# Performance work log

Measured on AMD Instinct MI355X. Metric: run time of the kernel, lower is better.

The kernel has to match this reference:

```python
import jax, jax.numpy as jnp
import numpy as np

N, F, M, B = 100000, 256, 10, 32768
DECAY = 0.9


def setup_inputs() -> dict:
    key = jax.random.key(0)
    ks = jax.random.split(key, 16)
    s = 1.0 / np.sqrt(F)
    # forward args
    node_indices = jax.random.permutation(ks[0], N)[:B]  # unique indices
    node_features = jax.random.normal(ks[1], (B, F), jnp.float32)
    # per-node state
    hidden_states = jax.random.normal(ks[2], (N, F), jnp.float32) * 0.1
    cell_states = jax.random.normal(ks[3], (N, F), jnp.float32) * 0.1
    temporal_memory = jax.random.normal(ks[4], (N, M, F), jnp.float32) * 0.1
    memory_ptr = jax.random.randint(ks[5], (N,), 0, M)
    # LSTMCell params (gate order i, f, g, o as in torch)
    W_ih = jax.random.normal(ks[6], (4 * F, F), jnp.float32) * s
    W_hh = jax.random.normal(ks[7], (4 * F, F), jnp.float32) * s
    b_ih = jax.random.normal(ks[8], (4 * F,), jnp.float32) * s
    b_hh = jax.random.normal(ks[9], (4 * F,), jnp.float32) * s
    # attention read params
    Wq = jax.random.normal(ks[10], (F, F), jnp.float32) * s
    bq = jnp.zeros((F,), jnp.float32)
    Wk = jax.random.normal(ks[11], (F, F), jnp.float32) * s
    bk = jnp.zeros((F,), jnp.float32)
    Wv = jax.random.normal(ks[12], (F, F), jnp.float32) * s
    bv = jnp.zeros((F,), jnp.float32)
    return dict(node_indices=node_indices, node_features=node_features,
                hidden_states=hidden_states, cell_states=cell_states,
                temporal_memory=temporal_memory, memory_ptr=memory_ptr,
                W_ih=W_ih, W_hh=W_hh, b_ih=b_ih, b_hh=b_hh,
                Wq=Wq, bq=bq, Wk=Wk, bk=bk, Wv=Wv, bv=bv)


def reference(node_indices, node_features, hidden_states, cell_states,
              temporal_memory, memory_ptr, W_ih, W_hh, b_ih, b_hh,
              Wq, bq, Wk, bk, Wv, bv):
    idx = node_indices
    feat = node_features.shape[-1]
    # --- update_memory: LSTMCell on gathered per-node states ---
    h_prev = hidden_states[idx]              # (B, F)
    c_prev = cell_states[idx]                # (B, F)
    gates = node_features @ W_ih.T + b_ih + h_prev @ W_hh.T + b_hh
    i, f, g, o = jnp.split(gates, 4, axis=-1)
    c_new = jax.nn.sigmoid(f) * c_prev + jax.nn.sigmoid(i) * jnp.tanh(g)
    h_new = jax.nn.sigmoid(o) * jnp.tanh(c_new)
    # --- scatter into circular temporal memory + decay previous slot ---
    ptr = memory_ptr[idx]                    # (B,)
    tm = temporal_memory.at[idx, ptr].set(node_features)
    prev = ptr - 1                           # -1 wraps; decay only applied if ptr > 0
    old = tm[idx, prev]                      # (B, F)
    tm = tm.at[idx, prev].set(jnp.where((ptr > 0)[:, None], old * DECAY, old))
    # --- get_temporal_context: gather + tiny attention over M slots ---
    mem = tm[idx]                            # (B, M, F)
    q = h_new @ Wq.T + bq                    # (B, F)  hidden_states[idx] post-update == h_new
    k = mem @ Wk.T + bk                      # (B, M, F)
    v = mem @ Wv.T + bv                      # (B, M, F)
    scores = jnp.einsum('bf,bmf->bm', q, k) / jnp.sqrt(jnp.asarray(feat, q.dtype))
    w = jax.nn.softmax(scores, axis=-1)      # (B, M)
    context = jnp.einsum('bmf,bm->bf', v, w) # (B, F)
    return context
```

## Files before the change

kernel.cpp:

```cpp
#include <hip/hip_runtime.h>
#include <hip/hip_bf16.h>

constexpr int NB = 32768;
constexpr int NF = 256;
constexpr int NM = 10;
constexpr float DECAY = 0.9f;

using bf16x8 = __attribute__((ext_vector_type(8))) short;
using f32x4  = __attribute__((ext_vector_type(4))) float;

static __device__ __forceinline__ ushort f2bf(float x) {
    unsigned u = __float_as_uint(x);
    unsigned r = (u + 0x7fffu + ((u >> 16) & 1u)) >> 16;
    return (ushort)r;
}
static __device__ __forceinline__ float bf2f(ushort x) {
    return __uint_as_float(((unsigned)x) << 16);
}
static __device__ __forceinline__ float sigmoid_f(float x) {
    return 1.f / (1.f + __expf(-x));
}
static __device__ __forceinline__ float tanh_f(float x) {
    float e = __expf(2.f * x);
    return (e - 1.f) / (e + 1.f);
}
static __device__ __forceinline__ void gload16(const void* g, void* l) {
    __builtin_amdgcn_global_load_lds(
        (const __attribute__((address_space(1))) unsigned int*)g,
        (__attribute__((address_space(3))) unsigned int*)l, 16, 0, 0);
}


__global__ void k_build_wgi(const float* __restrict__ W_ih, const float* __restrict__ W_hh,
                            const float* __restrict__ b_ih, const float* __restrict__ b_hh,
                            ushort* __restrict__ Wgi, float* __restrict__ bsum) {
    int j = blockIdx.x;
    int f = j >> 2, g = j & 3;
    int sr = g * 256 + f;
    for (int c = threadIdx.x; c < 512; c += 256) {
        float v = (c < 256) ? W_ih[sr * 256 + c] : W_hh[sr * 256 + (c - 256)];
        Wgi[j * 512 + c] = f2bf(v);
    }
    if (threadIdx.x == 0) bsum[j] = b_ih[sr] + b_hh[sr];
}

__global__ void k_build_wqkt(const float* __restrict__ Wq, const float* __restrict__ Wk,
                             ushort* __restrict__ WqkT) {
    int i = blockIdx.x, a = threadIdx.x;
    float s = 0.f;
#pragma unroll 8
    for (int j = 0; j < 256; ++j) s += Wq[j * 256 + a] * Wk[j * 256 + i];
    WqkT[i * 256 + a] = f2bf(s * 0.0625f);
}

__global__ void k_build_bqk(const float* __restrict__ bq, const float* __restrict__ Wk,
                            float* __restrict__ bqk) {
    int i = threadIdx.x;
    float s = 0.f;
#pragma unroll 8
    for (int j = 0; j < 256; ++j) s += bq[j] * Wk[j * 256 + i];
    bqk[i] = s * 0.0625f;
}

__global__ void k_conv_wv(const float* __restrict__ Wv, ushort* __restrict__ Wvb) {
    int t = blockIdx.x * 256 + threadIdx.x;
    Wvb[t] = f2bf(Wv[t]);
}

__global__ void k_build_acat(const float* __restrict__ nf, const float* __restrict__ hidden,
                             const int* __restrict__ idx, ushort* __restrict__ Acat) {
    int t = blockIdx.x * 256 + threadIdx.x;
    int row = t >> 7;
    int c4 = (t & 127) * 4;
    const float* src = (c4 < 256) ? (nf + (long)row * 256 + c4)
                                  : (hidden + (long)idx[row] * 256 + (c4 - 256));
    float4 v = *reinterpret_cast<const float4*>(src);
    ushort4 o;
    o.x = f2bf(v.x); o.y = f2bf(v.y); o.z = f2bf(v.z); o.w = f2bf(v.w);
    *reinterpret_cast<ushort4*>(Acat + (long)row * 512 + c4) = o;
}

__global__ __launch_bounds__(256) void k_gates2(
    const ushort* __restrict__ Acat, const ushort* __restrict__ Wgi,
    const float* __restrict__ bsum, const int* __restrict__ idx,
    const float* __restrict__ cell, ushort* __restrict__ h_new)
{
    __shared__ ushort As[128 * 32];
    __shared__ ushort Bs[128 * 32];
    const int t = threadIdx.x;
    const int w = t >> 6, l = t & 63;
    const int wr = w >> 1, wc = w & 1;
    const int lr = l & 15, lk = l >> 4;
    const int row0 = blockIdx.x * 128;
    const int col0 = blockIdx.y * 128;

    f32x4 acc[4][4];
#pragma unroll
    for (int m = 0; m < 4; ++m)
#pragma unroll
        for (int n = 0; n < 4; ++n) acc[m][n] = f32x4{0.f, 0.f, 0.f, 0.f};

    const int srow = l >> 2;
    const int scol = (l & 3) * 8;
    const int u0 = w * 2, u1 = u0 + 1;
    const ushort* aS0 = Acat + (size_t)(row0 + u0 * 16 + srow) * 512 + scol;
    const ushort* aS1 = Acat + (size_t)(row0 + u1 * 16 + srow) * 512 + scol;
    const ushort* bS0 = Wgi  + (size_t)(col0 + u0 * 16 + srow) * 512 + scol;
    const ushort* bS1 = Wgi  + (size_t)(col0 + u1 * 16 + srow) * 512 + scol;
    ushort* aL0 = As + u0 * 512; ushort* aL1 = As + u1 * 512;
    ushort* bL0 = Bs + u0 * 512; ushort* bL1 = Bs + u1 * 512;

    for (int k0 = 0; k0 < 512; k0 += 32) {
        gload16(aS0 + k0, aL0);
        gload16(aS1 + k0, aL1);
        gload16(bS0 + k0, bL0);
        gload16(bS1 + k0, bL1);
        __syncthreads();
        bf16x8 af[4], bfr[4];
#pragma unroll
        for (int m = 0; m < 4; ++m)
            af[m] = *reinterpret_cast<const bf16x8*>(As + (wr * 64 + m * 16 + lr) * 32 + lk * 8);
#pragma unroll
        for (int n = 0; n < 4; ++n)
            bfr[n] = *reinterpret_cast<const bf16x8*>(Bs + (wc * 64 + n * 16 + lr) * 32 + lk * 8);
#pragma unroll
        for (int m = 0; m < 4; ++m)
#pragma unroll
            for (int n = 0; n < 4; ++n)
                acc[m][n] = __builtin_amdgcn_mfma_f32_16x16x32_bf16(af[m], bfr[n], acc[m][n], 0, 0, 0);
        __syncthreads();
    }

    float bb[4];
#pragma unroll
    for (int n = 0; n < 4; ++n) bb[n] = bsum[col0 + wc * 64 + n * 16 + lr];
#pragma unroll
    for (int m = 0; m < 4; ++m)
#pragma unroll
        for (int n = 0; n < 4; ++n)
#pragma unroll
            for (int r = 0; r < 4; ++r) acc[m][n][r] += bb[n];

    const int g0 = lr & 3;
    const int fq = lr >> 2;
    const bool is0 = (g0 == 0), is1 = (g0 == 1), is2 = (g0 == 2), is3 = (g0 == 3);
    const int fbase = (col0 >> 2) + wc * 16;

    int nodev[4];
#pragma unroll
    for (int r = 0; r < 4; ++r)
        nodev[r] = idx[row0 + wr * 64 + g0 * 16 + lk * 4 + r];

#pragma unroll
    for (int n = 0; n < 4; ++n) {
#pragma unroll
        for (int r = 0; r < 4; ++r) {
            float own = is0 ? acc[0][n][r] : is1 ? acc[1][n][r] : is2 ? acc[2][n][r] : acc[3][n][r];
            float s1  = is0 ? acc[1][n][r] : is1 ? acc[0][n][r] : is2 ? acc[3][n][r] : acc[2][n][r];
            float s2  = is0 ? acc[2][n][r] : is1 ? acc[3][n][r] : is2 ? acc[0][n][r] : acc[1][n][r];
            float s3  = is0 ? acc[3][n][r] : is1 ? acc[2][n][r] : is2 ? acc[1][n][r] : acc[0][n][r];
            float r1 = __shfl_xor(s1, 1, 64);
            float r2 = __shfl_xor(s2, 2, 64);
            float r3 = __shfl_xor(s3, 3, 64);
            float gi = is0 ? own : is1 ? r1 : is2 ? r2 : r3;
            float gf = is1 ? own : is0 ? r1 : is3 ? r2 : r3;
            float gg = is2 ? own : is3 ? r1 : is0 ? r2 : r3;
            float go = is3 ? own : is2 ? r1 : is1 ? r2 : r3;
            int fg = fbase + n * 4 + fq;
            float cp = cell[(size_t)nodev[r] * 256 + fg];
            float cn = sigmoid_f(gf) * cp + sigmoid_f(gi) * tanh_f(gg);
            float hn = sigmoid_f(go) * tanh_f(cn);
            int grow = row0 + wr * 64 + g0 * 16 + lk * 4 + r;
            h_new[(size_t)grow * 256 + fg] = f2bf(hn);
        }
    }
}

static __device__ __forceinline__ int swzb(int row, int byteInRow) {
    return (row * 512 + byteInRow) ^ ((row & 7) << 4);
}

__global__ __launch_bounds__(256) void k_tail(
    const ushort* __restrict__ hnew, const ushort* __restrict__ WqkT,
    const float* __restrict__ bqk, const ushort* __restrict__ Wvb,
    const float* __restrict__ bv,
    const int* __restrict__ idx, const int* __restrict__ mptr,
    const float* __restrict__ tm, const float* __restrict__ nf,
    float* __restrict__ out)
{
    __shared__ ushort sQ[64 * 256];
    const int t = threadIdx.x, w = t >> 6, l = t & 63;
    const int lr = l & 15, lk = l >> 4;
    const int row0 = blockIdx.x * 64;
    char* sB = (char*)sQ;

    f32x4 acc[4][4];
#pragma unroll
    for (int m = 0; m < 4; ++m)
#pragma unroll
        for (int n = 0; n < 4; ++n) acc[m][n] = f32x4{0.f, 0.f, 0.f, 0.f};

    const ushort* aptr[4];
#pragma unroll
    for (int m = 0; m < 4; ++m) aptr[m] = hnew + (size_t)(row0 + m * 16 + lr) * 256 + lk * 8;
    const ushort* bptr[4];
#pragma unroll
    for (int n = 0; n < 4; ++n) bptr[n] = WqkT + (size_t)(w * 64 + n * 16 + lr) * 256 + lk * 8;

#pragma unroll 2
    for (int k = 0; k < 256; k += 32) {
        bf16x8 a[4], b[4];
#pragma unroll
        for (int m = 0; m < 4; ++m) a[m] = *reinterpret_cast<const bf16x8*>(aptr[m] + k);
#pragma unroll
        for (int n = 0; n < 4; ++n) b[n] = *reinterpret_cast<const bf16x8*>(bptr[n] + k);
#pragma unroll
        for (int m = 0; m < 4; ++m)
#pragma unroll
            for (int n = 0; n < 4; ++n)
                acc[m][n] = __builtin_amdgcn_mfma_f32_16x16x32_bf16(a[m], b[n], acc[m][n], 0, 0, 0);
    }
#pragma unroll
    for (int m = 0; m < 4; ++m)
#pragma unroll
        for (int n = 0; n < 4; ++n) {
            int colc = w * 64 + n * 16 + lr;
            float bbq = bqk[colc];
#pragma unroll
            for (int r = 0; r < 4; ++r) {
                int row = m * 16 + lk * 4 + r;
                *(ushort*)(sB + swzb(row, colc * 2)) = f2bf(acc[m][n][r] + bbq);
            }
        }
    __syncthreads();

    for (int rr = 0; rr < 16; ++rr) {
        int row = w * 16 + rr;
        int b = row0 + row;
        int node = idx[b];
        int ptr = mptr[node];
        ushort4 q4 = *(const ushort4*)(sB + swzb(row, l * 8));
        float q0 = bf2f(q4.x), q1 = bf2f(q4.y), q2 = bf2f(q4.z), q3 = bf2f(q4.w);
        const float* base = tm + (size_t)node * (NM * NF);

        float4 mem[NM];
        float sc[NM];
#pragma unroll
        for (int m = 0; m < NM; ++m) {
            float4 v;
            if (m == ptr) {
                v = *reinterpret_cast<const float4*>(nf + (size_t)b * 256 + l * 4);
            } else {
                v = *reinterpret_cast<const float4*>(base + (size_t)m * 256 + l * 4);
                if (ptr > 0 && m == ptr - 1) { v.x *= DECAY; v.y *= DECAY; v.z *= DECAY; v.w *= DECAY; }
            }
            mem[m] = v;
            sc[m] = q0 * v.x + q1 * v.y + q2 * v.z + q3 * v.w;
        }
#pragma unroll
        for (int m = 0; m < NM; ++m) {
            float s = sc[m];
#pragma unroll
            for (int d = 1; d < 64; d <<= 1) s += __shfl_xor(s, d, 64);
            sc[m] = s;
        }
        float mx = sc[0];
#pragma unroll
        for (int m = 1; m < NM; ++m) mx = fmaxf(mx, sc[m]);
        float e[NM], sum = 0.f;
#pragma unroll
        for (int m = 0; m < NM; ++m) { e[m] = __expf(sc[m] - mx); sum += e[m]; }
        float inv = 1.f / sum;

        float4 c = {0.f, 0.f, 0.f, 0.f};
#pragma unroll
        for (int m = 0; m < NM; ++m) {
            float wm = e[m] * inv;
            c.x += wm * mem[m].x; c.y += wm * mem[m].y; c.z += wm * mem[m].z; c.w += wm * mem[m].w;
        }
        ushort4 o;
        o.x = f2bf(c.x); o.y = f2bf(c.y); o.z = f2bf(c.z); o.w = f2bf(c.w);
        *(ushort4*)(sB + swzb(row, l * 8)) = o;
    }
    __syncthreads();

#pragma unroll
    for (int m = 0; m < 4; ++m)
#pragma unroll
        for (int n = 0; n < 4; ++n) acc[m][n] = f32x4{0.f, 0.f, 0.f, 0.f};
    const ushort* vptr[4];
#pragma unroll
    for (int n = 0; n < 4; ++n) vptr[n] = Wvb + (size_t)(w * 64 + n * 16 + lr) * 256 + lk * 8;

#pragma unroll 2
    for (int k = 0; k < 256; k += 32) {
        bf16x8 a[4], b[4];
#pragma unroll
        for (int m = 0; m < 4; ++m)
            a[m] = *reinterpret_cast<const bf16x8*>(sB + swzb(m * 16 + lr, (k + lk * 8) * 2));
#pragma unroll
        for (int n = 0; n < 4; ++n) b[n] = *reinterpret_cast<const bf16x8*>(vptr[n] + k);
#pragma unroll
        for (int m = 0; m < 4; ++m)
#pragma unroll
            for (int n = 0; n < 4; ++n)
                acc[m][n] = __builtin_amdgcn_mfma_f32_16x16x32_bf16(a[m], b[n], acc[m][n], 0, 0, 0);
    }
#pragma unroll
    for (int m = 0; m < 4; ++m)
#pragma unroll
        for (int n = 0; n < 4; ++n) {
            int colc = w * 64 + n * 16 + lr;
            float bbv = bv[colc];
#pragma unroll
            for (int r = 0; r < 4; ++r) {
                int row = m * 16 + lk * 4 + r;
                out[(size_t)(row0 + row) * 256 + colc] = acc[m][n][r] + bbv;
            }
        }
}

extern "C" void kernel_launch(void* const* d_in, const int* in_sizes, int n_in,
                              void* d_out, int out_size, void* d_ws, size_t ws_size,
                              hipStream_t stream) {
    const int*   node_indices = (const int*)  d_in[0];
    const float* node_feats   = (const float*)d_in[1];
    const float* hidden       = (const float*)d_in[2];
    const float* cell         = (const float*)d_in[3];
    const float* tmem         = (const float*)d_in[4];
    const int*   memory_ptr   = (const int*)  d_in[5];
    const float* W_ih         = (const float*)d_in[6];
    const float* W_hh         = (const float*)d_in[7];
    const float* b_ih         = (const float*)d_in[8];
    const float* b_hh         = (const float*)d_in[9];
    const float* Wq           = (const float*)d_in[10];
    const float* bq           = (const float*)d_in[11];
    const float* Wk           = (const float*)d_in[12];
    const float* Wv           = (const float*)d_in[14];
    const float* bv           = (const float*)d_in[15];

    char* ws = (char*)d_ws;
    size_t off = 0;
    auto alloc = [&](size_t bytes) { char* p = ws + off; off += (bytes + 255) & ~(size_t)255; return p; };

    ushort* Wgi   = (ushort*)alloc((size_t)1024 * 512 * 2);
    ushort* WqkT  = (ushort*)alloc((size_t)256 * 256 * 2);
    ushort* Wvb   = (ushort*)alloc((size_t)256 * 256 * 2);
    float*  bqk   = (float*) alloc((size_t)256 * 4);
    float*  bsum  = (float*) alloc((size_t)1024 * 4);
    ushort* Acat  = (ushort*)alloc((size_t)NB * 512 * 2);
    ushort* hnew  = (ushort*)alloc((size_t)NB * 256 * 2);

    k_build_wgi <<<1024, 256, 0, stream>>>(W_ih, W_hh, b_ih, b_hh, Wgi, bsum);
    k_build_wqkt<<<256, 256, 0, stream>>>(Wq, Wk, WqkT);
    k_build_bqk <<<1, 256, 0, stream>>>(bq, Wk, bqk);
    k_conv_wv   <<<256, 256, 0, stream>>>(Wv, Wvb);
    k_build_acat<<<NB * 128 / 256, 256, 0, stream>>>(node_feats, hidden, node_indices, Acat);

    k_gates2<<<dim3(NB / 128, 8), 256, 0, stream>>>(Acat, Wgi, bsum, node_indices, cell, hnew);
    k_tail  <<<NB / 64, 256, 0, stream>>>(hnew, WqkT, bqk, Wvb, bv,
                                          node_indices, memory_ptr, tmem, node_feats,
                                          (float*)d_out);
}
```

Before: 224.2 us.

## Merge prep kernels into one launch and halve tail kernel rows per block

Fuses the five preprocessing kernels (weight conversions, Wq·Wk fold, bias fold, Acat gather) into a single block-dispatched kernel, cutting launch overhead. The tail kernel now processes 32 rows per block instead of 64. That doubles the grid for more occupancy and latency hiding on the gather-heavy attention stage, and halves shared memory. Node indices and memory pointers are now prefetched per wave before the attention loop. The trade-off is that the Wqk and Wv weight tiles are reloaded twice as often across blocks.

```diff
diff --git a/kernel.cpp b/kernel.cpp
--- a/kernel.cpp
+++ b/kernel.cpp
@@ -30,54 +30,59 @@
         (__attribute__((address_space(3))) unsigned int*)l, 16, 0, 0);
 }
 
-
-__global__ void k_build_wgi(const float* __restrict__ W_ih, const float* __restrict__ W_hh,
-                            const float* __restrict__ b_ih, const float* __restrict__ b_hh,
-                            ushort* __restrict__ Wgi, float* __restrict__ bsum) {
-    int j = blockIdx.x;
-    int f = j >> 2, g = j & 3;
-    int sr = g * 256 + f;
-    for (int c = threadIdx.x; c < 512; c += 256) {
-        float v = (c < 256) ? W_ih[sr * 256 + c] : W_hh[sr * 256 + (c - 256)];
-        Wgi[j * 512 + c] = f2bf(v);
-    }
-    if (threadIdx.x == 0) bsum[j] = b_ih[sr] + b_hh[sr];
-}
-
-__global__ void k_build_wqkt(const float* __restrict__ Wq, const float* __restrict__ Wk,
-                             ushort* __restrict__ WqkT) {
-    int i = blockIdx.x, a = threadIdx.x;
-    float s = 0.f;
+constexpr int PB_ACAT = 16384;
+constexpr int PB_WGI  = PB_ACAT + 1024;
+constexpr int PB_WQKT = PB_WGI + 256;
+constexpr int PB_WV   = PB_WQKT + 256;
+constexpr int PB_TOT  = PB_WV + 1;
+
+__global__ __launch_bounds__(256) void k_prep(
+    const float* __restrict__ W_ih, const float* __restrict__ W_hh,
+    const float* __restrict__ b_ih, const float* __restrict__ b_hh,
+    const float* __restrict__ Wq, const float* __restrict__ bq,
+    const float* __restrict__ Wk, const float* __restrict__ Wv,
+    const float* __restrict__ nf, const float* __restrict__ hidden,
+    const int* __restrict__ idx,
+    ushort* __restrict__ Wgi, float* __restrict__ bsum,
+    ushort* __restrict__ WqkT, float* __restrict__ bqk,
+    ushort* __restrict__ Wvb, ushort* __restrict__ Acat)
+{
+    const int blk = blockIdx.x, tid = threadIdx.x;
+    if (blk < PB_ACAT) {
+        int t = blk * 256 + tid;
+        int row = t >> 7;
+        int c4 = (t & 127) * 4;
+        const float* src = (c4 < 256) ? (nf + (size_t)row * 256 + c4)
+                                      : (hidden + (size_t)idx[row] * 256 + (c4 - 256));
+        float4 v = *reinterpret_cast<const float4*>(src);
+        ushort4 o;
+        o.x = f2bf(v.x); o.y = f2bf(v.y); o.z = f2bf(v.z); o.w = f2bf(v.w);
+        *reinterpret_cast<ushort4*>(Acat + (size_t)row * 512 + c4) = o;
+    } else if (blk < PB_WGI) {
+        int j = blk - PB_ACAT;
+        int f = j >> 2, g = j & 3;
+        int sr = g * 256 + f;
+        for (int c = tid; c < 512; c += 256) {
+            float v = (c < 256) ? W_ih[sr * 256 + c] : W_hh[sr * 256 + (c - 256)];
+            Wgi[j * 512 + c] = f2bf(v);
+        }
+        if (tid == 0) bsum[j] = b_ih[sr] + b_hh[sr];
+    } else if (blk < PB_WQKT) {
+        int i = blk - PB_WGI, a = tid;
+        float s = 0.f;
 #pragma unroll 8
-    for (int j = 0; j < 256; ++j) s += Wq[j * 256 + a] * Wk[j * 256 + i];
-    WqkT[i * 256 + a] = f2bf(s * 0.0625f);
-}
-
-__global__ void k_build_bqk(const float* __restrict__ bq, const float* __restrict__ Wk,
-                            float* __restrict__ bqk) {
-    int i = threadIdx.x;
-    float s = 0.f;
+        for (int j = 0; j < 256; ++j) s += Wq[j * 256 + a] * Wk[j * 256 + i];
+        WqkT[i * 256 + a] = f2bf(s * 0.0625f);
+    } else if (blk < PB_WV) {
+        int t = (blk - PB_WQKT) * 256 + tid;
+        Wvb[t] = f2bf(Wv[t]);
+    } else {
+        int i = tid;
+        float s = 0.f;
 #pragma unroll 8
-    for (int j = 0; j < 256; ++j) s += bq[j] * Wk[j * 256 + i];
-    bqk[i] = s * 0.0625f;
-}
-
-__global__ void k_conv_wv(const float* __restrict__ Wv, ushort* __restrict__ Wvb) {
-    int t = blockIdx.x * 256 + threadIdx.x;
-    Wvb[t] = f2bf(Wv[t]);
-}
-
-__global__ void k_build_acat(const float* __restrict__ nf, const float* __restrict__ hidden,
-                             const int* __restrict__ idx, ushort* __restrict__ Acat) {
-    int t = blockIdx.x * 256 + threadIdx.x;
-    int row = t >> 7;
-    int c4 = (t & 127) * 4;
-    const float* src = (c4 < 256) ? (nf + (long)row * 256 + c4)
-                                  : (hidden + (long)idx[row] * 256 + (c4 - 256));
-    float4 v = *reinterpret_cast<const float4*>(src);
-    ushort4 o;
-    o.x = f2bf(v.x); o.y = f2bf(v.y); o.z = f2bf(v.z); o.w = f2bf(v.w);
-    *reinterpret_cast<ushort4*>(Acat + (long)row * 512 + c4) = o;
+        for (int j = 0; j < 256; ++j) s += bq[j] * Wk[j * 256 + i];
+        bqk[i] = s * 0.0625f;
+    }
 }
 
 __global__ __launch_bounds__(256) void k_gates2(
@@ -188,40 +193,40 @@
     const float* __restrict__ tm, const float* __restrict__ nf,
     float* __restrict__ out)
 {
-    __shared__ ushort sQ[64 * 256];
+    __shared__ ushort sQ[32 * 256];
     const int t = threadIdx.x, w = t >> 6, l = t & 63;
     const int lr = l & 15, lk = l >> 4;
-    const int row0 = blockIdx.x * 64;
+    const int row0 = blockIdx.x * 32;
     char* sB = (char*)sQ;
 
-    f32x4 acc[4][4];
-#pragma unroll
-    for (int m = 0; m < 4; ++m)
+    f32x4 acc[2][4];
+#pragma unroll
+    for (int m = 0; m < 2; ++m)
 #pragma unroll
         for (int n = 0; n < 4; ++n) acc[m][n] = f32x4{0.f, 0.f, 0.f, 0.f};
 
-    const ushort* aptr[4];
-#pragma unroll
-    for (int m = 0; m < 4; ++m) aptr[m] = hnew + (size_t)(row0 + m * 16 + lr) * 256 + lk * 8;
+    const ushort* aptr[2];
+#pragma unroll
+    for (int m = 0; m < 2; ++m) aptr[m] = hnew + (size_t)(row0 + m * 16 + lr) * 256 + lk * 8;
     const ushort* bptr[4];
 #pragma unroll
     for (int n = 0; n < 4; ++n) bptr[n] = WqkT + (size_t)(w * 64 + n * 16 + lr) * 256 + lk * 8;
 
 #pragma unroll 2
     for (int k = 0; k < 256; k += 32) {
-        bf16x8 a[4], b[4];
-#pragma unroll
-        for (int m = 0; m < 4; ++m) a[m] = *reinterpret_cast<const bf16x8*>(aptr[m] + k);
+        bf16x8 a[2], b[4];
+#pragma unroll
+        for (int m = 0; m < 2; ++m) a[m] = *reinterpret_cast<const bf16x8*>(aptr[m] + k);
 #pragma unroll
         for (int n = 0; n < 4; ++n) b[n] = *reinterpret_cast<const bf16x8*>(bptr[n] + k);
 #pragma unroll
-        for (int m = 0; m < 4; ++m)
+        for (int m = 0; m < 2; ++m)
 #pragma unroll
             for (int n = 0; n < 4; ++n)
                 acc[m][n] = __builtin_amdgcn_mfma_f32_16x16x32_bf16(a[m], b[n], acc[m][n], 0, 0, 0);
     }
 #pragma unroll
-    for (int m = 0; m < 4; ++m)
+    for (int m = 0; m < 2; ++m)
 #pragma unroll
         for (int n = 0; n < 4; ++n) {
             int colc = w * 64 + n * 16 + lr;
@@ -234,58 +239,66 @@
         }
     __syncthreads();
 
-    for (int rr = 0; rr < 16; ++rr) {
-        int row = w * 16 + rr;
-        int b = row0 + row;
-        int node = idx[b];
-        int ptr = mptr[node];
-        ushort4 q4 = *(const ushort4*)(sB + swzb(row, l * 8));
-        float q0 = bf2f(q4.x), q1 = bf2f(q4.y), q2 = bf2f(q4.z), q3 = bf2f(q4.w);
-        const float* base = tm + (size_t)node * (NM * NF);
-
-        float4 mem[NM];
-        float sc[NM];
-#pragma unroll
-        for (int m = 0; m < NM; ++m) {
-            float4 v;
-            if (m == ptr) {
-                v = *reinterpret_cast<const float4*>(nf + (size_t)b * 256 + l * 4);
-            } else {
-                v = *reinterpret_cast<const float4*>(base + (size_t)m * 256 + l * 4);
-                if (ptr > 0 && m == ptr - 1) { v.x *= DECAY; v.y *= DECAY; v.z *= DECAY; v.w *= DECAY; }
-            }
-            mem[m] = v;
-            sc[m] = q0 * v.x + q1 * v.y + q2 * v.z + q3 * v.w;
-        }
-#pragma unroll
-        for (int m = 0; m < NM; ++m) {
-            float s = sc[m];
-#pragma unroll
-            for (int d = 1; d < 64; d <<= 1) s += __shfl_xor(s, d, 64);
-            sc[m] = s;
-        }
-        float mx = sc[0];
-#pragma unroll
-        for (int m = 1; m < NM; ++m) mx = fmaxf(mx, sc[m]);
-        float e[NM], sum = 0.f;
-#pragma unroll
-        for (int m = 0; m < NM; ++m) { e[m] = __expf(sc[m] - mx); sum += e[m]; }
-        float inv = 1.f / sum;
-
-        float4 c = {0.f, 0.f, 0.f, 0.f};
-#pragma unroll
-        for (int m = 0; m < NM; ++m) {
-            float wm = e[m] * inv;
-            c.x += wm * mem[m].x; c.y += wm * mem[m].y; c.z += wm * mem[m].z; c.w += wm * mem[m].w;
-        }
-        ushort4 o;
-        o.x = f2bf(c.x); o.y = f2bf(c.y); o.z = f2bf(c.z); o.w = f2bf(c.w);
-        *(ushort4*)(sB + swzb(row, l * 8)) = o;
+    {
+        const int b0 = row0 + w * 8;
+        int nodes[8], ptrs[8];
+#pragma unroll
+        for (int r = 0; r < 8; ++r) { nodes[r] = idx[b0 + r]; ptrs[r] = mptr[nodes[r]]; }
+
+#pragma unroll 2
+        for (int rr = 0; rr < 8; ++rr) {
+            int row = w * 8 + rr;
+            int b = b0 + rr;
+            int node = nodes[rr];
+            int ptr = ptrs[rr];
+            ushort4 q4 = *(const ushort4*)(sB + swzb(row, l * 8));
+            float q0 = bf2f(q4.x), q1 = bf2f(q4.y), q2 = bf2f(q4.z), q3 = bf2f(q4.w);
+            const float* base = tm + (size_t)node * (NM * NF);
+
+            float4 mem[NM];
+            float sc[NM];
+#pragma unroll
+            for (int m = 0; m < NM; ++m) {
+                float4 v;
+                if (m == ptr) {
+                    v = *reinterpret_cast<const float4*>(nf + (size_t)b * 256 + l * 4);
+                } else {
+                    v = *reinterpret_cast<const float4*>(base + (size_t)m * 256 + l * 4);
+                    if (ptr > 0 && m == ptr - 1) { v.x *= DECAY; v.y *= DECAY; v.z *= DECAY; v.w *= DECAY; }
+                }
+                mem[m] = v;
+                sc[m] = q0 * v.x + q1 * v.y + q2 * v.z + q3 * v.w;
+            }
+#pragma unroll
+            for (int m = 0; m < NM; ++m) {
+                float s = sc[m];
+#pragma unroll
+                for (int d = 1; d < 64; d <<= 1) s += __shfl_xor(s, d, 64);
+                sc[m] = s;
+            }
+            float mx = sc[0];
+#pragma unroll
+            for (int m = 1; m < NM; ++m) mx = fmaxf(mx, sc[m]);
+            float e[NM], sum = 0.f;
+#pragma unroll
+            for (int m = 0; m < NM; ++m) { e[m] = __expf(sc[m] - mx); sum += e[m]; }
+            float inv = 1.f / sum;
+
+            float4 c = {0.f, 0.f, 0.f, 0.f};
+#pragma unroll
+            for (int m = 0; m < NM; ++m) {
+                float wm = e[m] * inv;
+                c.x += wm * mem[m].x; c.y += wm * mem[m].y; c.z += wm * mem[m].z; c.w += wm * mem[m].w;
+            }
+            ushort4 o;
+            o.x = f2bf(c.x); o.y = f2bf(c.y); o.z = f2bf(c.z); o.w = f2bf(c.w);
+            *(ushort4*)(sB + swzb(row, l * 8)) = o;
+        }
     }
     __syncthreads();
 
 #pragma unroll
-    for (int m = 0; m < 4; ++m)
+    for (int m = 0; m < 2; ++m)
 #pragma unroll
         for (int n = 0; n < 4; ++n) acc[m][n] = f32x4{0.f, 0.f, 0.f, 0.f};
     const ushort* vptr[4];
@@ -294,20 +307,20 @@
 
 #pragma unroll 2
     for (int k = 0; k < 256; k += 32) {
-        bf16x8 a[4], b[4];
-#pragma unroll
-        for (int m = 0; m < 4; ++m)
+        bf16x8 a[2], b[4];
+#pragma unroll
+        for (int m = 0; m < 2; ++m)
             a[m] = *reinterpret_cast<const bf16x8*>(sB + swzb(m * 16 + lr, (k + lk * 8) * 2));
 #pragma unroll
         for (int n = 0; n < 4; ++n) b[n] = *reinterpret_cast<const bf16x8*>(vptr[n] + k);
 #pragma unroll
-        for (int m = 0; m < 4; ++m)
+        for (int m = 0; m < 2; ++m)
 #pragma unroll
             for (int n = 0; n < 4; ++n)
                 acc[m][n] = __builtin_amdgcn_mfma_f32_16x16x32_bf16(a[m], b[n], acc[m][n], 0, 0, 0);
     }
 #pragma unroll
-    for (int m = 0; m < 4; ++m)
+    for (int m = 0; m < 2; ++m)
 #pragma unroll
         for (int n = 0; n < 4; ++n) {
             int colc = w * 64 + n * 16 + lr;
@@ -351,14 +364,11 @@
     ushort* Acat  = (ushort*)alloc((size_t)NB * 512 * 2);
     ushort* hnew  = (ushort*)alloc((size_t)NB * 256 * 2);
 
-    k_build_wgi <<<1024, 256, 0, stream>>>(W_ih, W_hh, b_ih, b_hh, Wgi, bsum);
-    k_build_wqkt<<<256, 256, 0, stream>>>(Wq, Wk, WqkT);
-    k_build_bqk <<<1, 256, 0, stream>>>(bq, Wk, bqk);
-    k_conv_wv   <<<256, 256, 0, stream>>>(Wv, Wvb);
-    k_build_acat<<<NB * 128 / 256, 256, 0, stream>>>(node_feats, hidden, node_indices, Acat);
-
+    k_prep<<<PB_TOT, 256, 0, stream>>>(W_ih, W_hh, b_ih, b_hh, Wq, bq, Wk, Wv,
+                                       node_feats, hidden, node_indices,
+                                       Wgi, bsum, WqkT, bqk, Wvb, Acat);
     k_gates2<<<dim3(NB / 128, 8), 256, 0, stream>>>(Acat, Wgi, bsum, node_indices, cell, hnew);
-    k_tail  <<<NB / 64, 256, 0, stream>>>(hnew, WqkT, bqk, Wvb, bv,
-                                          node_indices, memory_ptr, tmem, node_feats,
-                                          (float*)d_out);
-}
+    k_tail<<<NB / 32, 256, 0, stream>>>(hnew, WqkT, bqk, Wvb, bv,
+                                        node_indices, memory_ptr, tmem, node_feats,
+                                        (float*)d_out);
+}
```

After: 223.5 us. Within noise of the previous version (-0.3%).
